# Performance work log

Measured on AMD Instinct MI355X. Metric: run time of the kernel, lower is better.

The kernel has to match this reference:

```python
import jax, jax.numpy as jnp
import numpy as np

B, S, H = 2, 1024, 2880
I = 2880
E = 16
K = 4


def setup_inputs() -> dict:
    key = jax.random.key(0)
    ks = jax.random.split(key, 4)
    sc = 0.02  # init scale to keep activations in a sane range
    return {
        "x": jax.random.normal(ks[0], (B, S, H), jnp.float32),
        "gate_w": jax.random.normal(ks[1], (E, H), jnp.float32) * sc,
        "gate_b": jnp.zeros((E,), jnp.float32),
        "w_gate_up": jax.random.normal(ks[2], (E, 2 * I, H), jnp.float32) * sc,
        "b_gate_up": jnp.zeros((E, 2 * I), jnp.float32),
        "w_down": jax.random.normal(ks[3], (E, H, I), jnp.float32) * sc,
        "b_down": jnp.zeros((E, H), jnp.float32),
        "swiglu_alpha": jnp.full((E,), 1.702, jnp.float32),
        "swiglu_beta": jnp.full((E,), 1.0, jnp.float32),
        "swiglu_limit": jnp.full((E,), 7.0, jnp.float32),
    }


def reference(x, gate_w, gate_b, w_gate_up, b_gate_up, w_down, b_down,
              swiglu_alpha, swiglu_beta, swiglu_limit):
    orig_shape = x.shape
    hidden = orig_shape[-1]
    t = x.reshape(-1, hidden)  # [T, H]
    T = t.shape[0]

    # Router: gate linear -> top-k -> renormalize via softmax over selected logits
    logits = t @ gate_w.T + gate_b  # [T, E]
    top_vals, top_idx = jax.lax.top_k(logits, K)  # [T, K]
    top_w = jax.nn.softmax(top_vals, axis=-1)  # RenormalizeMoeRoutingMethod
    # Dense combine matrix [T, E]; zero for non-selected experts
    combine = jnp.zeros((T, E), t.dtype).at[jnp.arange(T)[:, None], top_idx].set(top_w)

    def expert_body(acc, params):
        wgu, bgu, wd, bd, alpha, beta, lim, cw = params
        h = t @ wgu.T + bgu  # [T, 2I] fused gate_up
        glu, lin = jnp.split(h, 2, axis=-1)  # FUSED_GATE_UP_PROJ chunk
        glu = jnp.minimum(glu, lim)  # swiglu_limit clamp (gpt-oss)
        lin = jnp.clip(lin, -lim, lim)
        act = glu * jax.nn.sigmoid(alpha * glu) * (lin + beta)  # [T, I]
        y = act @ wd.T + bd  # [T, H]
        return acc + cw[:, None] * y, None

    init = jnp.zeros((T, hidden), t.dtype)
    out, _ = jax.lax.scan(
        expert_body, init,
        (w_gate_up, b_gate_up, w_down, b_down,
         swiglu_alpha, swiglu_beta, swiglu_limit, combine.T))
    return out.reshape(orig_shape)
```

## Files before the change

kernel.cpp:

```cpp
#include <hip/hip_runtime.h>
#include <stdint.h>
#include <math.h>

#define T_TOK 2048
#define H_DIM 2880
#define I_DIM 2880
#define E_NUM 16
#define TOPK 4

#define BT 128
#define BK 32
#define NK 90
#define MT_MAX 16
#define NT1 45
#define NT2 45

typedef __bf16 bf16_t;
typedef __bf16 bf16x8 __attribute__((ext_vector_type(8)));
typedef __bf16 bf16x4 __attribute__((ext_vector_type(4)));
typedef float f32x4 __attribute__((ext_vector_type(4)));

#define WAITV(N) asm volatile("s_waitcnt vmcnt(" #N ")" ::: "memory")
#define WAITL()  asm volatile("s_waitcnt lgkmcnt(0)" ::: "memory")
#define BAR()    asm volatile("s_barrier" ::: "memory")

__device__ __forceinline__ void gload16(const bf16_t* g, bf16_t* l) {
  __builtin_amdgcn_global_load_lds(
      (__attribute__((address_space(1))) const uint32_t*)g,
      (__attribute__((address_space(3))) uint32_t*)l, 16, 0, 0);
}

__device__ __forceinline__ f32x4 mfma16(bf16x8 a, bf16x8 b, f32x4 c) {
  return __builtin_amdgcn_mfma_f32_16x16x32_bf16(a, b, c, 0, 0, 0);
}

__device__ __forceinline__ int ldsoff(int row, int g) {
  int r = row & 31;
  return ((row >> 5) << 10) + (((r << 2) + ((g + (r >> 1)) & 3)) << 3);
}

__global__ void k_prep(const float* __restrict__ x, bf16_t* __restrict__ xbf,
                       int* __restrict__ counts) {
  if (blockIdx.x == 0 && threadIdx.x < E_NUM) counts[threadIdx.x] = 0;
  int idx = blockIdx.x * 256 + threadIdx.x;
  const int total = T_TOK * H_DIM / 8;
  if (idx < total) {
    f32x4 a = ((const f32x4*)x)[2 * idx];
    f32x4 b = ((const f32x4*)x)[2 * idx + 1];
    bf16x8 o = {(bf16_t)a[0], (bf16_t)a[1], (bf16_t)a[2], (bf16_t)a[3],
                (bf16_t)b[0], (bf16_t)b[1], (bf16_t)b[2], (bf16_t)b[3]};
    ((bf16x8*)xbf)[idx] = o;
  }
}

__global__ void k_router(const float* __restrict__ x, const float* __restrict__ gw,
                         const float* __restrict__ gb, float* __restrict__ topw,
                         int* __restrict__ counts, int* __restrict__ rowsl) {
  const int t = blockIdx.x;
  const int lane = threadIdx.x;
  const int c = lane >> 4, e = lane & 15;
  const f32x4* x4 = (const f32x4*)(x + (size_t)t * H_DIM);
  const f32x4* w4 = (const f32x4*)(gw + (size_t)e * H_DIM);
  float p = 0.f;
  const int per = (H_DIM / 4) / 4;
  for (int i = c * per; i < (c + 1) * per; ++i) {
    f32x4 xv = x4[i], wv = w4[i];
    p += xv[0] * wv[0] + xv[1] * wv[1] + xv[2] * wv[2] + xv[3] * wv[3];
  }
  p += __shfl_xor(p, 16);
  p += __shfl_xor(p, 32);
  p += gb[e];
  __shared__ float lg[E_NUM];
  if (lane < E_NUM) lg[lane] = p;
  __syncthreads();
  if (lane == 0) {
    float v[E_NUM];
    #pragma unroll
    for (int i = 0; i < E_NUM; ++i) v[i] = lg[i];
    int idxs[TOPK]; float vals[TOPK];
    for (int k = 0; k < TOPK; ++k) {
      int bi = 0; float bv = -1e30f;
      for (int i = 0; i < E_NUM; ++i) {
        if (v[i] > bv) { bv = v[i]; bi = i; }
      }
      idxs[k] = bi; vals[k] = bv; v[bi] = -1e30f;
    }
    float m = vals[0], s = 0.f, w[TOPK];
    for (int k = 0; k < TOPK; ++k) { w[k] = expf(vals[k] - m); s += w[k]; }
    for (int k = 0; k < TOPK; ++k) {
      int slot = t * TOPK + k;
      topw[slot] = w[k] / s;
      int pos = atomicAdd(&counts[idxs[k]], 1);
      rowsl[idxs[k] * T_TOK + pos] = slot;
    }
  }
}

#define G_STAGE_T(KT, BUF) do {                                         \
    int c1_ = (KT) > (NK - 1) ? (NK - 1) : (KT);                        \
    _Pragma("unroll")                                                   \
    for (int i_ = 0; i_ < 2; ++i_)                                      \
      gload16(tsrc[i_] + c1_ * BK, &sT[BUF][wv * 1024 + i_ * 512]);     \
  } while (0)


#define G1_MFMA(SWC, STR) do {                                          \
    const int g_ = lane >> 4, rs_ = lane & 15;                          \
    bf16x8 wg_[2], wl_[2], tf[4];                                       \
    _Pragma("unroll")                                                   \
    for (int wi = 0; wi < 2; ++wi) {                                    \
      int rg = 32 * wm + 16 * wi + rs_;                                 \
      wg_[wi] = *(const bf16x8*)(&sW[SWC][ldsoff(rg, g_)]);             \
      wl_[wi] = *(const bf16x8*)(&sW[SWC][ldsoff(rg + 64, g_)]);        \
    }                                                                   \
    _Pragma("unroll")                                                   \
    for (int tj = 0; tj < 4; ++tj) {                                    \
      int rt = 64 * wt + 16 * tj + rs_;                                 \
      tf[tj] = *(const bf16x8*)(&sT[STR][ldsoff(rt, g_)]);              \
    }                                                                   \
    _Pragma("unroll")                                                   \
    for (int wi = 0; wi < 2; ++wi)                                      \
      _Pragma("unroll")                                                 \
      for (int tj = 0; tj < 4; ++tj) {                                  \
        accg[wi][tj] = mfma16(wg_[wi], tf[tj], accg[wi][tj]);           \
        accl[wi][tj] = mfma16(wl_[wi], tf[tj], accl[wi][tj]);           \
      }                                                                 \
  } while (0)

#define G1_ITER(KK, WSET, SWC, STR, STW) do {                           \
    G_STAGE_T((KK) + 2, STW);                                           \
    _Pragma("unroll")                                                   \
    for (int p_ = 0; p_ < 4; ++p_) {                                    \
      bf16x4 b_ = {(bf16_t)WSET[p_][0], (bf16_t)WSET[p_][1],            \
                   (bf16_t)WSET[p_][2], (bf16_t)WSET[p_][3]};           \
      *(bf16x4*)(&sW[(SWC) ^ 1][wo[p_]]) = b_;                          \
    }                                                                   \
    { int c3_ = (KK) + 3 > (NK - 1) ? (NK - 1) : (KK) + 3;              \
      _Pragma("unroll")                                                 \
      for (int p_ = 0; p_ < 4; ++p_)                                    \
        WSET[p_] = *(const f32x4*)(wbase + wgo[p_] + c3_ * BK); }       \
    __builtin_amdgcn_s_setprio(1);                                      \
    G1_MFMA(SWC, STR);                                                  \
    __builtin_amdgcn_s_setprio(0);                                      \
    WAITV(6); WAITL(); BAR();                                           \
  } while (0)

__global__ __launch_bounds__(256, 2)
void k_gemm1(const bf16_t* __restrict__ xbf, const float* __restrict__ wgu,
             const float* __restrict__ bgu, const float* __restrict__ al,
             const float* __restrict__ be, const float* __restrict__ lim_,
             const int* __restrict__ counts, const int* __restrict__ rowsl,
             bf16_t* __restrict__ act) {
  const int nwg = E_NUM * NT1 * MT_MAX;
  const int L = (blockIdx.x & 7) * (nwg >> 3) + (blockIdx.x >> 3);
  const int mt = L & (MT_MAX - 1);
  const int t2 = L >> 4;
  const int nt = t2 % NT1;
  const int e  = t2 / NT1;
  const int Ne = counts[e];
  const int m0 = mt * BT;
  if (m0 >= Ne) return;
  const int n0 = nt * 64;

  __shared__ alignas(16) bf16_t sW[2][128 * 32];
  __shared__ alignas(16) bf16_t sT[3][128 * 32];

  const int tid = threadIdx.x;
  const int wv = tid >> 6, lane = tid & 63;
  const int wm = wv & 1, wt = wv >> 1;
  const int* rl = rowsl + e * T_TOK;

  const bf16_t* tsrc[2];
  {
    #pragma unroll
    for (int i = 0; i < 2; ++i) {
      int q = i * 64 + lane;
      int r = q >> 2;
      int g = ((q & 3) - (r >> 1)) & 3;
      int li = m0 + wv * 32 + r; if (li > Ne - 1) li = Ne - 1;
      int tok = rl[li] >> 2;
      tsrc[i] = xbf + (size_t)tok * H_DIM + g * 8;
    }
  }

  const int wrow = tid >> 3, wf2 = tid & 7;
  const float* wbase = wgu + (size_t)e * (2 * I_DIM) * H_DIM + wf2 * 4;
  int wgo[4], wo[4];
  #pragma unroll
  for (int p = 0; p < 4; ++p) {
    int row = wrow + p * 32;
    int grow = (row < 64) ? (n0 + row) : (I_DIM + n0 + row - 64);
    wgo[p] = grow * H_DIM;
    wo[p] = ldsoff(row, wf2 >> 1) + (wf2 & 1) * 4;
  }

  f32x4 zero = {0.f, 0.f, 0.f, 0.f};
  f32x4 accg[2][4], accl[2][4];
  #pragma unroll
  for (int i = 0; i < 2; ++i)
    #pragma unroll
    for (int j = 0; j < 4; ++j) { accg[i][j] = zero; accl[i][j] = zero; }

  f32x4 wA[4], wB[4];
  #pragma unroll
  for (int p = 0; p < 4; ++p) wA[p] = *(const f32x4*)(wbase + wgo[p]);
  WAITV(0);
  #pragma unroll
  for (int p = 0; p < 4; ++p) {
    bf16x4 b = {(bf16_t)wA[p][0], (bf16_t)wA[p][1],
                (bf16_t)wA[p][2], (bf16_t)wA[p][3]};
    *(bf16x4*)(&sW[0][wo[p]]) = b;
  }
  G_STAGE_T(0, 0);
  #pragma unroll
  for (int p = 0; p < 4; ++p) wA[p] = *(const f32x4*)(wbase + wgo[p] + BK);
  WAITV(0);
  G_STAGE_T(1, 1);
  #pragma unroll
  for (int p = 0; p < 4; ++p) wB[p] = *(const f32x4*)(wbase + wgo[p] + 2 * BK);
  WAITL(); BAR();

  for (int kb = 0; kb < NK; kb += 6) {
    G1_ITER(kb + 0, wA, 0, 0, 2);
    G1_ITER(kb + 1, wB, 1, 1, 0);
    G1_ITER(kb + 2, wA, 0, 2, 1);
    G1_ITER(kb + 3, wB, 1, 0, 2);
    G1_ITER(kb + 4, wA, 0, 1, 0);
    G1_ITER(kb + 5, wB, 1, 2, 1);
  }

  const float alpha = al[e], beta = be[e], lim = lim_[e];
  const float* bgp = bgu + (size_t)e * (2 * I_DIM);
  #pragma unroll
  for (int wi = 0; wi < 2; ++wi) {
    const int nb = n0 + 32 * wm + 16 * wi + ((lane >> 4) << 2);
    f32x4 bg4 = *(const f32x4*)(bgp + nb);
    f32x4 bl4 = *(const f32x4*)(bgp + I_DIM + nb);
    #pragma unroll
    for (int tj = 0; tj < 4; ++tj) {
      const int li2 = m0 + 64 * wt + 16 * tj + (lane & 15);
      if (li2 < Ne) {
        const int slot = rl[li2];
        bf16x4 ov;
        #pragma unroll
        for (int r = 0; r < 4; ++r) {
          float g = accg[wi][tj][r] + bg4[r];
          float l = accl[wi][tj][r] + bl4[r];
          g = fminf(g, lim);
          l = fminf(fmaxf(l, -lim), lim);
          float sg = 1.0f / (1.0f + expf(-alpha * g));
          ov[r] = (bf16_t)(g * sg * (l + beta));
        }
        *(bf16x4*)(&act[(size_t)slot * I_DIM + nb]) = ov;
      }
    }
  }
}


#define G2_MFMA(SWC, STR) do {                                          \
    const int g_ = lane >> 4, rs_ = lane & 15;                          \
    bf16x8 wf_[2], tf[4];                                               \
    _Pragma("unroll")                                                   \
    for (int wi = 0; wi < 2; ++wi) {                                    \
      int rg = 32 * wm + 16 * wi + rs_;                                 \
      wf_[wi] = *(const bf16x8*)(&sW[SWC][ldsoff(rg, g_)]);             \
    }                                                                   \
    _Pragma("unroll")                                                   \
    for (int tj = 0; tj < 4; ++tj) {                                    \
      int rt = 64 * wt + 16 * tj + rs_;                                 \
      tf[tj] = *(const bf16x8*)(&sT[STR][ldsoff(rt, g_)]);              \
    }                                                                   \
    _Pragma("unroll")                                                   \
    for (int wi = 0; wi < 2; ++wi)                                      \
      _Pragma("unroll")                                                 \
      for (int tj = 0; tj < 4; ++tj)                                    \
        acc[wi][tj] = mfma16(wf_[wi], tf[tj], acc[wi][tj]);             \
  } while (0)

#define G2_ITER(KK, WSET, SWC, STR, STW) do {                           \
    G_STAGE_T((KK) + 2, STW);                                           \
    _Pragma("unroll")                                                   \
    for (int p_ = 0; p_ < 2; ++p_) {                                    \
      bf16x4 b_ = {(bf16_t)WSET[p_][0], (bf16_t)WSET[p_][1],            \
                   (bf16_t)WSET[p_][2], (bf16_t)WSET[p_][3]};           \
      *(bf16x4*)(&sW[(SWC) ^ 1][wo[p_]]) = b_;                          \
    }                                                                   \
    { int c3_ = (KK) + 3 > (NK - 1) ? (NK - 1) : (KK) + 3;              \
      _Pragma("unroll")                                                 \
      for (int p_ = 0; p_ < 2; ++p_)                                    \
        WSET[p_] = *(const f32x4*)(wbase + wgo[p_] + c3_ * BK); }       \
    __builtin_amdgcn_s_setprio(1);                                      \
    G2_MFMA(SWC, STR);                                                  \
    __builtin_amdgcn_s_setprio(0);                                      \
    WAITV(4); WAITL(); BAR();                                           \
  } while (0)

__global__ __launch_bounds__(256, 2)
void k_gemm2(const bf16_t* __restrict__ act, const float* __restrict__ wd,
             const float* __restrict__ bd, const float* __restrict__ topw,
             const int* __restrict__ counts, const int* __restrict__ rowsl,
             float* __restrict__ ybuf) {
  const int nwg = E_NUM * NT2 * MT_MAX;
  const int L = (blockIdx.x & 7) * (nwg >> 3) + (blockIdx.x >> 3);
  const int mt = L & (MT_MAX - 1);
  const int t2 = L >> 4;
  const int ht = t2 % NT2;
  const int e  = t2 / NT2;
  const int Ne = counts[e];
  const int m0 = mt * BT;
  if (m0 >= Ne) return;
  const int h0 = ht * 64;

  __shared__ alignas(16) bf16_t sW[2][64 * 32];
  __shared__ alignas(16) bf16_t sT[3][128 * 32];

  const int tid = threadIdx.x;
  const int wv = tid >> 6, lane = tid & 63;
  const int wm = wv & 1, wt = wv >> 1;
  const int* rl = rowsl + e * T_TOK;

  const bf16_t* tsrc[2];
  {
    #pragma unroll
    for (int i = 0; i < 2; ++i) {
      int q = i * 64 + lane;
      int r = q >> 2;
      int g = ((q & 3) - (r >> 1)) & 3;
      int li = m0 + wv * 32 + r; if (li > Ne - 1) li = Ne - 1;
      int slot = rl[li];
      tsrc[i] = act + (size_t)slot * I_DIM + g * 8;
    }
  }

  const int wrow = tid >> 3, wf2 = tid & 7;
  const float* wbase = wd + (size_t)e * H_DIM * I_DIM + wf2 * 4;
  int wgo[2], wo[2];
  #pragma unroll
  for (int p = 0; p < 2; ++p) {
    int row = wrow + p * 32;
    wgo[p] = (h0 + row) * I_DIM;
    wo[p] = ldsoff(row, wf2 >> 1) + (wf2 & 1) * 4;
  }

  f32x4 zero = {0.f, 0.f, 0.f, 0.f};
  f32x4 acc[2][4];
  #pragma unroll
  for (int i = 0; i < 2; ++i)
    #pragma unroll
    for (int j = 0; j < 4; ++j) acc[i][j] = zero;

  f32x4 wA[2], wB[2];
  #pragma unroll
  for (int p = 0; p < 2; ++p) wA[p] = *(const f32x4*)(wbase + wgo[p]);
  WAITV(0);
  #pragma unroll
  for (int p = 0; p < 2; ++p) {
    bf16x4 b = {(bf16_t)wA[p][0], (bf16_t)wA[p][1],
                (bf16_t)wA[p][2], (bf16_t)wA[p][3]};
    *(bf16x4*)(&sW[0][wo[p]]) = b;
  }
  G_STAGE_T(0, 0);
  #pragma unroll
  for (int p = 0; p < 2; ++p) wA[p] = *(const f32x4*)(wbase + wgo[p] + BK);
  WAITV(0);
  G_STAGE_T(1, 1);
  #pragma unroll
  for (int p = 0; p < 2; ++p) wB[p] = *(const f32x4*)(wbase + wgo[p] + 2 * BK);
  WAITL(); BAR();

  for (int kb = 0; kb < NK; kb += 6) {
    G2_ITER(kb + 0, wA, 0, 0, 2);
    G2_ITER(kb + 1, wB, 1, 1, 0);
    G2_ITER(kb + 2, wA, 0, 2, 1);
    G2_ITER(kb + 3, wB, 1, 0, 2);
    G2_ITER(kb + 4, wA, 0, 1, 0);
    G2_ITER(kb + 5, wB, 1, 2, 1);
  }

  const float* bdp = bd + (size_t)e * H_DIM;
  #pragma unroll
  for (int wi = 0; wi < 2; ++wi) {
    const int hb = h0 + 32 * wm + 16 * wi + ((lane >> 4) << 2);
    f32x4 b4 = *(const f32x4*)(bdp + hb);
    #pragma unroll
    for (int tj = 0; tj < 4; ++tj) {
      const int li2 = m0 + 64 * wt + 16 * tj + (lane & 15);
      if (li2 < Ne) {
        const int slot = rl[li2];
        const float tw = topw[slot];
        f32x4 o = (acc[wi][tj] + b4) * tw;
        *(f32x4*)(&ybuf[(size_t)slot * H_DIM + hb]) = o;
      }
    }
  }
}

__global__ void k_combine(const float* __restrict__ ybuf, float* __restrict__ out) {
  const int j4 = H_DIM / 4;
  int idx = blockIdx.x * 256 + threadIdx.x;
  if (idx >= T_TOK * j4) return;
  int t = idx / j4, j = idx - t * j4;
  const f32x4* yb = (const f32x4*)ybuf;
  f32x4 s = yb[(size_t)(t * 4 + 0) * j4 + j];
  s = s + yb[(size_t)(t * 4 + 1) * j4 + j];
  s = s + yb[(size_t)(t * 4 + 2) * j4 + j];
  s = s + yb[(size_t)(t * 4 + 3) * j4 + j];
  ((f32x4*)out)[idx] = s;
}

extern "C" void kernel_launch(void* const* d_in, const int* in_sizes, int n_in,
                              void* d_out, int out_size, void* d_ws, size_t ws_size,
                              hipStream_t stream) {
  const float* x   = (const float*)d_in[0];
  const float* gw  = (const float*)d_in[1];
  const float* gb  = (const float*)d_in[2];
  const float* wgu = (const float*)d_in[3];
  const float* bgu = (const float*)d_in[4];
  const float* wd  = (const float*)d_in[5];
  const float* bd  = (const float*)d_in[6];
  const float* sal = (const float*)d_in[7];
  const float* sbe = (const float*)d_in[8];
  const float* sli = (const float*)d_in[9];
  float* out = (float*)d_out;

  char* ws = (char*)d_ws;
  int*    counts = (int*)(ws + 0);
  int*    rowsl  = (int*)(ws + 4096);
  float*  topw   = (float*)(ws + 4096 + 131072);
  bf16_t* xbf    = (bf16_t*)(ws + (1 << 20));
  bf16_t* act    = (bf16_t*)(ws + (size_t)(16 << 20));
  float*  ybuf   = (float*)(ws + (size_t)(64 << 20));

  k_prep<<<dim3(2880), dim3(256), 0, stream>>>(x, xbf, counts);
  k_router<<<dim3(T_TOK), dim3(64), 0, stream>>>(x, gw, gb, topw, counts, rowsl);
  k_gemm1<<<dim3(E_NUM * NT1 * MT_MAX), dim3(256), 0, stream>>>(
      xbf, wgu, bgu, sal, sbe, sli, counts, rowsl, act);
  k_gemm2<<<dim3(E_NUM * NT2 * MT_MAX), dim3(256), 0, stream>>>(
      act, wd, bd, topw, counts, rowsl, ybuf);
  k_combine<<<dim3(5760), dim3(256), 0, stream>>>(ybuf, out);
}
```

Baseline: 1.648 ms.

## Stage fp32 expert weights directly to LDS via global_load_lds and convert at read

Both expert GEMMs now stream fp32 weight tiles straight into LDS with global_load_lds using an XOR-swizzled layout, instead of loading them into registers, converting to bf16, and storing to LDS. The fp32-to-bf16 conversion moves to the fragment read just before the MFMA. This is meant to free VGPRs, remove the register round trip and ds_write traffic, and simplify the pipeline waits. The cost is twice the LDS footprint and read bandwidth for weights and repeated conversion work per wave. k_gemm2 launch bounds are raised to 3 blocks per CU to add occupancy.

```diff
diff --git a/kernel.cpp b/kernel.cpp
--- a/kernel.cpp
+++ b/kernel.cpp
@@ -24,7 +24,7 @@
 #define WAITL()  asm volatile("s_waitcnt lgkmcnt(0)" ::: "memory")
 #define BAR()    asm volatile("s_barrier" ::: "memory")
 
-__device__ __forceinline__ void gload16(const bf16_t* g, bf16_t* l) {
+__device__ __forceinline__ void gload16(const void* g, void* l) {
   __builtin_amdgcn_global_load_lds(
       (__attribute__((address_space(1))) const uint32_t*)g,
       (__attribute__((address_space(3))) uint32_t*)l, 16, 0, 0);
@@ -37,6 +37,15 @@
 __device__ __forceinline__ int ldsoff(int row, int g) {
   int r = row & 31;
   return ((row >> 5) << 10) + (((r << 2) + ((g + (r >> 1)) & 3)) << 3);
+}
+__device__ __forceinline__ int swoff(int row, int G) {
+  return row * 32 + (((G) ^ (row & 7)) << 2);
+}
+
+__device__ __forceinline__ bf16x8 cvt8(f32x4 a, f32x4 b) {
+  bf16x8 o = {(bf16_t)a[0], (bf16_t)a[1], (bf16_t)a[2], (bf16_t)a[3],
+              (bf16_t)b[0], (bf16_t)b[1], (bf16_t)b[2], (bf16_t)b[3]};
+  return o;
 }
 
 __global__ void k_prep(const float* __restrict__ x, bf16_t* __restrict__ xbf,
@@ -47,9 +56,7 @@
   if (idx < total) {
     f32x4 a = ((const f32x4*)x)[2 * idx];
     f32x4 b = ((const f32x4*)x)[2 * idx + 1];
-    bf16x8 o = {(bf16_t)a[0], (bf16_t)a[1], (bf16_t)a[2], (bf16_t)a[3],
-                (bf16_t)b[0], (bf16_t)b[1], (bf16_t)b[2], (bf16_t)b[3]};
-    ((bf16x8*)xbf)[idx] = o;
+    ((bf16x8*)xbf)[idx] = cvt8(a, b);
   }
 }
 
@@ -104,19 +111,30 @@
   } while (0)
 
 
+#define G1_STAGE_W(KT, BUF) do {                                        \
+    int cw_ = (KT) > (NK - 1) ? (NK - 1) : (KT);                        \
+    _Pragma("unroll")                                                   \
+    for (int i_ = 0; i_ < 4; ++i_)                                      \
+      gload16(wsrc[i_] + cw_ * BK, &sWf[BUF][(32 * wv + 8 * i_) * 32]); \
+  } while (0)
+
 #define G1_MFMA(SWC, STR) do {                                          \
-    const int g_ = lane >> 4, rs_ = lane & 15;                          \
+    const int u_ = lane >> 4, rs_ = lane & 15;                          \
     bf16x8 wg_[2], wl_[2], tf[4];                                       \
     _Pragma("unroll")                                                   \
     for (int wi = 0; wi < 2; ++wi) {                                    \
       int rg = 32 * wm + 16 * wi + rs_;                                 \
-      wg_[wi] = *(const bf16x8*)(&sW[SWC][ldsoff(rg, g_)]);             \
-      wl_[wi] = *(const bf16x8*)(&sW[SWC][ldsoff(rg + 64, g_)]);        \
+      f32x4 a0 = *(const f32x4*)(&sWf[SWC][swoff(rg, 2 * u_)]);         \
+      f32x4 a1 = *(const f32x4*)(&sWf[SWC][swoff(rg, 2 * u_ + 1)]);     \
+      wg_[wi] = cvt8(a0, a1);                                           \
+      f32x4 b0 = *(const f32x4*)(&sWf[SWC][swoff(rg + 64, 2 * u_)]);    \
+      f32x4 b1 = *(const f32x4*)(&sWf[SWC][swoff(rg + 64, 2 * u_ + 1)]);\
+      wl_[wi] = cvt8(b0, b1);                                           \
     }                                                                   \
     _Pragma("unroll")                                                   \
     for (int tj = 0; tj < 4; ++tj) {                                    \
       int rt = 64 * wt + 16 * tj + rs_;                                 \
-      tf[tj] = *(const bf16x8*)(&sT[STR][ldsoff(rt, g_)]);              \
+      tf[tj] = *(const bf16x8*)(&sT[STR][ldsoff(rt, u_)]);              \
     }                                                                   \
     _Pragma("unroll")                                                   \
     for (int wi = 0; wi < 2; ++wi)                                      \
@@ -127,22 +145,13 @@
       }                                                                 \
   } while (0)
 
-#define G1_ITER(KK, WSET, SWC, STR, STW) do {                           \
+#define G1_ITER(KK, SWC, STR, STW) do {                                 \
+    G1_STAGE_W((KK) + 1, (SWC) ^ 1);                                    \
     G_STAGE_T((KK) + 2, STW);                                           \
-    _Pragma("unroll")                                                   \
-    for (int p_ = 0; p_ < 4; ++p_) {                                    \
-      bf16x4 b_ = {(bf16_t)WSET[p_][0], (bf16_t)WSET[p_][1],            \
-                   (bf16_t)WSET[p_][2], (bf16_t)WSET[p_][3]};           \
-      *(bf16x4*)(&sW[(SWC) ^ 1][wo[p_]]) = b_;                          \
-    }                                                                   \
-    { int c3_ = (KK) + 3 > (NK - 1) ? (NK - 1) : (KK) + 3;              \
-      _Pragma("unroll")                                                 \
-      for (int p_ = 0; p_ < 4; ++p_)                                    \
-        WSET[p_] = *(const f32x4*)(wbase + wgo[p_] + c3_ * BK); }       \
     __builtin_amdgcn_s_setprio(1);                                      \
     G1_MFMA(SWC, STR);                                                  \
     __builtin_amdgcn_s_setprio(0);                                      \
-    WAITV(6); WAITL(); BAR();                                           \
+    WAITV(2); WAITL(); BAR();                                           \
   } while (0)
 
 __global__ __launch_bounds__(256, 2)
@@ -162,7 +171,7 @@
   if (m0 >= Ne) return;
   const int n0 = nt * 64;
 
-  __shared__ alignas(16) bf16_t sW[2][128 * 32];
+  __shared__ alignas(16) float  sWf[2][128 * 32];
   __shared__ alignas(16) bf16_t sT[3][128 * 32];
 
   const int tid = threadIdx.x;
@@ -183,15 +192,16 @@
     }
   }
 
-  const int wrow = tid >> 3, wf2 = tid & 7;
-  const float* wbase = wgu + (size_t)e * (2 * I_DIM) * H_DIM + wf2 * 4;
-  int wgo[4], wo[4];
-  #pragma unroll
-  for (int p = 0; p < 4; ++p) {
-    int row = wrow + p * 32;
-    int grow = (row < 64) ? (n0 + row) : (I_DIM + n0 + row - 64);
-    wgo[p] = grow * H_DIM;
-    wo[p] = ldsoff(row, wf2 >> 1) + (wf2 & 1) * 4;
+  const float* wsrc[4];
+  {
+    const int rloc = lane >> 3, g = lane & 7;
+    #pragma unroll
+    for (int i = 0; i < 4; ++i) {
+      int row = 32 * wv + 8 * i + rloc;
+      int grow = (row < 64) ? (n0 + row) : (I_DIM + n0 + row - 64);
+      wsrc[i] = wgu + (size_t)e * (2 * I_DIM) * H_DIM + (size_t)grow * H_DIM
+                + ((g ^ (row & 7)) << 2);
+    }
   }
 
   f32x4 zero = {0.f, 0.f, 0.f, 0.f};
@@ -201,32 +211,18 @@
     #pragma unroll
     for (int j = 0; j < 4; ++j) { accg[i][j] = zero; accl[i][j] = zero; }
 
-  f32x4 wA[4], wB[4];
-  #pragma unroll
-  for (int p = 0; p < 4; ++p) wA[p] = *(const f32x4*)(wbase + wgo[p]);
-  WAITV(0);
-  #pragma unroll
-  for (int p = 0; p < 4; ++p) {
-    bf16x4 b = {(bf16_t)wA[p][0], (bf16_t)wA[p][1],
-                (bf16_t)wA[p][2], (bf16_t)wA[p][3]};
-    *(bf16x4*)(&sW[0][wo[p]]) = b;
-  }
+  G1_STAGE_W(0, 0);
   G_STAGE_T(0, 0);
-  #pragma unroll
-  for (int p = 0; p < 4; ++p) wA[p] = *(const f32x4*)(wbase + wgo[p] + BK);
-  WAITV(0);
   G_STAGE_T(1, 1);
-  #pragma unroll
-  for (int p = 0; p < 4; ++p) wB[p] = *(const f32x4*)(wbase + wgo[p] + 2 * BK);
-  WAITL(); BAR();
+  WAITV(2); BAR();
 
   for (int kb = 0; kb < NK; kb += 6) {
-    G1_ITER(kb + 0, wA, 0, 0, 2);
-    G1_ITER(kb + 1, wB, 1, 1, 0);
-    G1_ITER(kb + 2, wA, 0, 2, 1);
-    G1_ITER(kb + 3, wB, 1, 0, 2);
-    G1_ITER(kb + 4, wA, 0, 1, 0);
-    G1_ITER(kb + 5, wB, 1, 2, 1);
+    G1_ITER(kb + 0, 0, 0, 2);
+    G1_ITER(kb + 1, 1, 1, 0);
+    G1_ITER(kb + 2, 0, 2, 1);
+    G1_ITER(kb + 3, 1, 0, 2);
+    G1_ITER(kb + 4, 0, 1, 0);
+    G1_ITER(kb + 5, 1, 2, 1);
   }
 
   const float alpha = al[e], beta = be[e], lim = lim_[e];
@@ -258,18 +254,27 @@
 }
 
 
+#define G2_STAGE_W(KT, BUF) do {                                        \
+    int cw_ = (KT) > (NK - 1) ? (NK - 1) : (KT);                        \
+    _Pragma("unroll")                                                   \
+    for (int i_ = 0; i_ < 2; ++i_)                                      \
+      gload16(wsrc[i_] + cw_ * BK, &sWf[BUF][(16 * wv + 8 * i_) * 32]); \
+  } while (0)
+
 #define G2_MFMA(SWC, STR) do {                                          \
-    const int g_ = lane >> 4, rs_ = lane & 15;                          \
+    const int u_ = lane >> 4, rs_ = lane & 15;                          \
     bf16x8 wf_[2], tf[4];                                               \
     _Pragma("unroll")                                                   \
     for (int wi = 0; wi < 2; ++wi) {                                    \
       int rg = 32 * wm + 16 * wi + rs_;                                 \
-      wf_[wi] = *(const bf16x8*)(&sW[SWC][ldsoff(rg, g_)]);             \
+      f32x4 a0 = *(const f32x4*)(&sWf[SWC][swoff(rg, 2 * u_)]);         \
+      f32x4 a1 = *(const f32x4*)(&sWf[SWC][swoff(rg, 2 * u_ + 1)]);     \
+      wf_[wi] = cvt8(a0, a1);                                           \
     }                                                                   \
     _Pragma("unroll")                                                   \
     for (int tj = 0; tj < 4; ++tj) {                                    \
       int rt = 64 * wt + 16 * tj + rs_;                                 \
-      tf[tj] = *(const bf16x8*)(&sT[STR][ldsoff(rt, g_)]);              \
+      tf[tj] = *(const bf16x8*)(&sT[STR][ldsoff(rt, u_)]);              \
     }                                                                   \
     _Pragma("unroll")                                                   \
     for (int wi = 0; wi < 2; ++wi)                                      \
@@ -278,25 +283,16 @@
         acc[wi][tj] = mfma16(wf_[wi], tf[tj], acc[wi][tj]);             \
   } while (0)
 
-#define G2_ITER(KK, WSET, SWC, STR, STW) do {                           \
+#define G2_ITER(KK, SWC, STR, STW) do {                                 \
+    G2_STAGE_W((KK) + 1, (SWC) ^ 1);                                    \
     G_STAGE_T((KK) + 2, STW);                                           \
-    _Pragma("unroll")                                                   \
-    for (int p_ = 0; p_ < 2; ++p_) {                                    \
-      bf16x4 b_ = {(bf16_t)WSET[p_][0], (bf16_t)WSET[p_][1],            \
-                   (bf16_t)WSET[p_][2], (bf16_t)WSET[p_][3]};           \
-      *(bf16x4*)(&sW[(SWC) ^ 1][wo[p_]]) = b_;                          \
-    }                                                                   \
-    { int c3_ = (KK) + 3 > (NK - 1) ? (NK - 1) : (KK) + 3;              \
-      _Pragma("unroll")                                                 \
-      for (int p_ = 0; p_ < 2; ++p_)                                    \
-        WSET[p_] = *(const f32x4*)(wbase + wgo[p_] + c3_ * BK); }       \
     __builtin_amdgcn_s_setprio(1);                                      \
     G2_MFMA(SWC, STR);                                                  \
     __builtin_amdgcn_s_setprio(0);                                      \
-    WAITV(4); WAITL(); BAR();                                           \
-  } while (0)
-
-__global__ __launch_bounds__(256, 2)
+    WAITV(2); WAITL(); BAR();                                           \
+  } while (0)
+
+__global__ __launch_bounds__(256, 3)
 void k_gemm2(const bf16_t* __restrict__ act, const float* __restrict__ wd,
              const float* __restrict__ bd, const float* __restrict__ topw,
              const int* __restrict__ counts, const int* __restrict__ rowsl,
@@ -312,7 +308,7 @@
   if (m0 >= Ne) return;
   const int h0 = ht * 64;
 
-  __shared__ alignas(16) bf16_t sW[2][64 * 32];
+  __shared__ alignas(16) float  sWf[2][64 * 32];
   __shared__ alignas(16) bf16_t sT[3][128 * 32];
 
   const int tid = threadIdx.x;
@@ -333,14 +329,15 @@
     }
   }
 
-  const int wrow = tid >> 3, wf2 = tid & 7;
-  const float* wbase = wd + (size_t)e * H_DIM * I_DIM + wf2 * 4;
-  int wgo[2], wo[2];
-  #pragma unroll
-  for (int p = 0; p < 2; ++p) {
-    int row = wrow + p * 32;
-    wgo[p] = (h0 + row) * I_DIM;
-    wo[p] = ldsoff(row, wf2 >> 1) + (wf2 & 1) * 4;
+  const float* wsrc[2];
+  {
+    const int rloc = lane >> 3, g = lane & 7;
+    #pragma unroll
+    for (int i = 0; i < 2; ++i) {
+      int row = 16 * wv + 8 * i + rloc;
+      wsrc[i] = wd + (size_t)e * H_DIM * I_DIM + (size_t)(h0 + row) * I_DIM
+                + ((g ^ (row & 7)) << 2);
+    }
   }
 
   f32x4 zero = {0.f, 0.f, 0.f, 0.f};
@@ -350,32 +347,18 @@
     #pragma unroll
     for (int j = 0; j < 4; ++j) acc[i][j] = zero;
 
-  f32x4 wA[2], wB[2];
-  #pragma unroll
-  for (int p = 0; p < 2; ++p) wA[p] = *(const f32x4*)(wbase + wgo[p]);
-  WAITV(0);
-  #pragma unroll
-  for (int p = 0; p < 2; ++p) {
-    bf16x4 b = {(bf16_t)wA[p][0], (bf16_t)wA[p][1],
-                (bf16_t)wA[p][2], (bf16_t)wA[p][3]};
-    *(bf16x4*)(&sW[0][wo[p]]) = b;
-  }
+  G2_STAGE_W(0, 0);
   G_STAGE_T(0, 0);
-  #pragma unroll
-  for (int p = 0; p < 2; ++p) wA[p] = *(const f32x4*)(wbase + wgo[p] + BK);
-  WAITV(0);
   G_STAGE_T(1, 1);
-  #pragma unroll
-  for (int p = 0; p < 2; ++p) wB[p] = *(const f32x4*)(wbase + wgo[p] + 2 * BK);
-  WAITL(); BAR();
+  WAITV(2); BAR();
 
   for (int kb = 0; kb < NK; kb += 6) {
-    G2_ITER(kb + 0, wA, 0, 0, 2);
-    G2_ITER(kb + 1, wB, 1, 1, 0);
-    G2_ITER(kb + 2, wA, 0, 2, 1);
-    G2_ITER(kb + 3, wB, 1, 0, 2);
-    G2_ITER(kb + 4, wA, 0, 1, 0);
-    G2_ITER(kb + 5, wB, 1, 2, 1);
+    G2_ITER(kb + 0, 0, 0, 2);
+    G2_ITER(kb + 1, 1, 1, 0);
+    G2_ITER(kb + 2, 0, 2, 1);
+    G2_ITER(kb + 3, 1, 0, 2);
+    G2_ITER(kb + 4, 0, 1, 0);
+    G2_ITER(kb + 5, 1, 2, 1);
   }
 
   const float* bdp = bd + (size_t)e * H_DIM;
```

After: 1.768 ms. 7.3% more time.
